# Kernel tuning notes

Hardware: AMD Instinct MI355X
Metric: run time of the kernel (lower is better)

## Reference

```python
import jax, jax.numpy as jnp
import numpy as np

B, S, N, C = 64, 512, 207, 1
H = 256
D = N * C          # flattened node-feature size (input_size * n_nodes)
DIN = 2 * D        # GRU input size with concat_mask=True


def setup_inputs() -> dict:
    key = jax.random.key(0)
    ks = jax.random.split(key, 8)
    x = jax.random.normal(ks[0], (B, S, N, C), dtype=jnp.float32)
    mask = (jax.random.uniform(ks[1], (B, S, N, C)) < 0.8).astype(jnp.float32)
    bnd = 1.0 / np.sqrt(H)  # torch default init bound for GRUCell and Linear(H, D)
    u = lambda k, shp: jax.random.uniform(k, shp, minval=-bnd, maxval=bnd, dtype=jnp.float32)
    return {
        'x': x,
        'mask': mask,
        'W_ih': u(ks[2], (3 * H, DIN)),
        'W_hh': u(ks[3], (3 * H, H)),
        'b_ih': u(ks[4], (3 * H,)),
        'b_hh': u(ks[5], (3 * H,)),
        'W_ro': u(ks[6], (D, H)),
        'b_ro': u(ks[7], (D,)),
    }


def _gru_cell(x_t, h, W_ih, W_hh, b_ih, b_hh):
    gi = x_t @ W_ih.T + b_ih              # [B, 3H]
    gh = h @ W_hh.T + b_hh                # [B, 3H]
    i_r, i_z, i_n = jnp.split(gi, 3, axis=-1)
    h_r, h_z, h_n = jnp.split(gh, 3, axis=-1)
    r = jax.nn.sigmoid(i_r + h_r)
    z = jax.nn.sigmoid(i_z + h_z)
    n = jnp.tanh(i_n + r * h_n)
    return (1.0 - z) * n + z * h


def reference(x, mask, W_ih, W_hh, b_ih, b_hh, W_ro, b_ro):
    b, s, n_nodes, c = x.shape
    xf = x.reshape(b, s, n_nodes * c)       # 'b s n c -> b s (n c)'
    mf = mask.reshape(b, s, n_nodes * c)
    h0 = jnp.zeros((b, H), dtype=x.dtype)   # state_init='zero'
    xhat0 = h0 @ W_ro.T + b_ro              # readout of initial state

    def step(carry, inp):
        h, x_hat = carry
        x_t, m_t = inp                       # [B, D] each
        x_p = jnp.where(m_t > 0.5, x_t, x_hat)
        x_in = jnp.concatenate([x_p, m_t], axis=-1)  # concat_mask
        h_new = _gru_cell(x_in, h, W_ih, W_hh, b_ih, b_hh)
        x_hat_new = h_new @ W_ro.T + b_ro
        return (h_new, x_hat_new), x_hat_new

    # scan over steps 0..S-2, time axis leading
    xs = (jnp.swapaxes(xf[:, :-1], 0, 1), jnp.swapaxes(mf[:, :-1], 0, 1))
    _, preds = jax.lax.scan(step, (h0, xhat0), xs)           # [S-1, B, D]
    preds = jnp.concatenate([xhat0[None], preds], axis=0)    # [S, B, D]
    x_hat = jnp.swapaxes(preds, 0, 1).reshape(b, s, n_nodes, c)
    return x_hat
```

## Files before the change

kernel.cpp:

```cpp
#include <hip/hip_runtime.h>
#include <math.h>

#define BB 64
#define SS 512
#define DD 207
#define HH 256
#define NWG 64
#define LDW 676
#define ROW 260
#define AG __HIP_MEMORY_SCOPE_AGENT

#define SROWS 672
#define HOFF  416
#define SLOT  (SROWS * 64)
#define BUF_FLOATS ((size_t)SS * SLOT)
#define FLAG_U32 (64 * 32)
#define STAGE_FLOATS ((size_t)SS * DD * 64)
#define WS_NEED6 ((BUF_FLOATS + FLAG_U32 + STAGE_FLOATS) * sizeof(float))

#define V3_AROWS 928
#define V3_HBASE 416
#define V3_ACT (V3_AROWS * 64)
#define V3_FLAGS (64 * 32)
#define V3_WS_SMALL ((size_t)(V3_ACT + V3_FLAGS) * sizeof(float))
#define V3_WS_FULL  ((size_t)(V3_ACT + V3_FLAGS + STAGE_FLOATS) * sizeof(float))

__device__ __forceinline__ void ast4(float* p, float v) {
    union { float f; unsigned u; } c; c.f = v;
    __hip_atomic_store((unsigned*)p, c.u, __ATOMIC_RELAXED, AG);
}

__device__ __forceinline__ void run_range6(
    const float4* __restrict__ A4, const float* __restrict__ wgl,
    float* __restrict__ red, int u, int bp, int wc0, int gr0, int len, int slot)
{
    float4 c0 = make_float4(0.f, 0.f, 0.f, 0.f);
    float4 c1 = c0, c2 = c0;
    #pragma unroll 4
    for (int k = 0; k < len; k += 4) {
        float4 a0 = A4[(gr0 + k + 0) * 16 + bp];
        float4 a1 = A4[(gr0 + k + 1) * 16 + bp];
        float4 a2 = A4[(gr0 + k + 2) * 16 + bp];
        float4 a3 = A4[(gr0 + k + 3) * 16 + bp];
        float4 w0 = *(const float4*)&wgl[(0 + u) * LDW + wc0 + k];
        float4 w1 = *(const float4*)&wgl[(4 + u) * LDW + wc0 + k];
        float4 w2 = *(const float4*)&wgl[(8 + u) * LDW + wc0 + k];
        c0.x += a0.x*w0.x + a1.x*w0.y + a2.x*w0.z + a3.x*w0.w;
        c0.y += a0.y*w0.x + a1.y*w0.y + a2.y*w0.z + a3.y*w0.w;
        c0.z += a0.z*w0.x + a1.z*w0.y + a2.z*w0.z + a3.z*w0.w;
        c0.w += a0.w*w0.x + a1.w*w0.y + a2.w*w0.z + a3.w*w0.w;
        c1.x += a0.x*w1.x + a1.x*w1.y + a2.x*w1.z + a3.x*w1.w;
        c1.y += a0.y*w1.x + a1.y*w1.y + a2.y*w1.z + a3.y*w1.w;
        c1.z += a0.z*w1.x + a1.z*w1.y + a2.z*w1.z + a3.z*w1.w;
        c1.w += a0.w*w1.x + a1.w*w1.y + a2.w*w1.z + a3.w*w1.w;
        c2.x += a0.x*w2.x + a1.x*w2.y + a2.x*w2.z + a3.x*w2.w;
        c2.y += a0.y*w2.x + a1.y*w2.y + a2.y*w2.z + a3.y*w2.w;
        c2.z += a0.z*w2.x + a1.z*w2.y + a2.z*w2.z + a3.z*w2.w;
        c2.w += a0.w*w2.x + a1.w*w2.y + a2.w*w2.z + a3.w*w2.w;
    }
    float4* R4 = (float4*)red;
    R4[(slot * 12 + 0 + u) * 16 + bp] = c0;
    R4[(slot * 12 + 4 + u) * 16 + bp] = c1;
    R4[(slot * 12 + 8 + u) * 16 + bp] = c2;
}

__global__ __launch_bounds__(256) void rnn_init6(float* __restrict__ ws) {
    int i = blockIdx.x * blockDim.x + threadIdx.x;
    for (int idx = i; idx < HH * 64; idx += gridDim.x * blockDim.x)
        ws[HOFF * 64 + idx] = 0.f;
    unsigned* fl = (unsigned*)(ws + BUF_FLOATS);
    for (int idx = i; idx < FLAG_U32; idx += gridDim.x * blockDim.x)
        fl[idx] = 0u;
}

__global__ __launch_bounds__(512) void rnn_persist7(
    const float* __restrict__ x, const float* __restrict__ mask,
    const float* __restrict__ W_ih, const float* __restrict__ W_hh,
    const float* __restrict__ b_ih, const float* __restrict__ b_hh,
    const float* __restrict__ W_ro, const float* __restrict__ b_ro,
    float* __restrict__ ws, float* __restrict__ out)
{
    const int wg = blockIdx.x;
    const int tid = threadIdx.x;
    const int lane = tid & 63;
    const int wv = tid >> 6;

    float* buf = ws;
    unsigned* flags = (unsigned*)(ws + BUF_FLOATS);
    float* stage = ws + BUF_FLOATS + FLAG_U32;

    __shared__ float wgl[12 * LDW];
    __shared__ float wrol[4 * ROW];
    __shared__ float red[16 * 12 * 64];
    __shared__ float redB[32 * 64];
    __shared__ float hloc[4 * 64];
    __shared__ float bihl[12], bhhl[12], brol[4];

    const int d0 = (207 * wg) / NWG;
    const int d1 = (207 * (wg + 1)) / NWG;
    const int dc = d1 - d0;

    for (int i = tid; i < 12 * LDW; i += 512) {
        int r = i / LDW, c = i - r * LDW;
        int rg = (r >> 2) * 256 + wg * 4 + (r & 3);
        float v = 0.f;
        if (c < 414) v = W_ih[rg * 414 + c];
        else if (c >= 416 && c < 672) v = W_hh[rg * 256 + (c - 416)];
        wgl[i] = v;
    }
    for (int i = tid; i < 4 * 256; i += 512) {
        int dl_ = i >> 8, j = i & 255;
        wrol[dl_ * ROW + j] = (dl_ < dc) ? W_ro[(d0 + dl_) * 256 + j] : 0.f;
    }
    if (tid < 12) {
        int rg = (tid >> 2) * 256 + wg * 4 + (tid & 3);
        bihl[tid] = b_ih[rg];
        bhhl[tid] = b_hh[rg];
    }
    if (tid < 4) brol[tid] = (tid < dc) ? b_ro[d0 + tid] : 0.f;
    if (tid < 256) hloc[tid] = 0.f;
    __syncthreads();

    const float4* A4 = (const float4*)buf;
    const int u  = lane >> 4;
    const int bp = lane & 15;

    const bool have = (tid < dc * 64);
    const int dl = tid >> 6, b = tid & 63;
    const size_t gbase = (size_t)b * (SS * DD) + (d0 + dl);
    float xv_pf = 0.f, mv_pf = 0.f;
    if (have) { xv_pf = x[gbase]; mv_pf = mask[gbase]; }

    unsigned gen = 0;

    for (int t = 0; t < SS; ++t) {
        const int sbase = t * SROWS;

        {
            const float* hrow = buf + (size_t)(sbase + HOFF) * 64;
            const int jb = wv * 32;
            float acc0 = 0.f, acc1 = 0.f, acc2 = 0.f, acc3 = 0.f;
            #pragma unroll 4
            for (int j = 0; j < 32; j += 4) {
                float a0 = hrow[(jb + j + 0) * 64 + lane];
                float a1 = hrow[(jb + j + 1) * 64 + lane];
                float a2 = hrow[(jb + j + 2) * 64 + lane];
                float a3 = hrow[(jb + j + 3) * 64 + lane];
                float4 w0 = *(const float4*)&wrol[0 * ROW + jb + j];
                float4 w1 = *(const float4*)&wrol[1 * ROW + jb + j];
                float4 w2 = *(const float4*)&wrol[2 * ROW + jb + j];
                float4 w3 = *(const float4*)&wrol[3 * ROW + jb + j];
                acc0 += a0*w0.x + a1*w0.y + a2*w0.z + a3*w0.w;
                acc1 += a0*w1.x + a1*w1.y + a2*w1.z + a3*w1.w;
                acc2 += a0*w2.x + a1*w2.y + a2*w2.z + a3*w2.w;
                acc3 += a0*w3.x + a1*w3.y + a2*w3.z + a3*w3.w;
            }
            redB[(wv * 4 + 0) * 64 + lane] = acc0;
            redB[(wv * 4 + 1) * 64 + lane] = acc1;
            redB[(wv * 4 + 2) * 64 + lane] = acc2;
            redB[(wv * 4 + 3) * 64 + lane] = acc3;
        }
        __syncthreads();
        if (have) {
            float xh = brol[dl];
            #pragma unroll
            for (int g = 0; g < 8; ++g)
                xh += redB[(g * 4 + dl) * 64 + b];
            stage[(t * DD + d0 + dl) * 64 + b] = xh;
            if (t < SS - 1) {
                float xi = (mv_pf > 0.5f) ? xv_pf : xh;
                ast4(&buf[(size_t)(sbase + d0 + dl) * 64 + b], xi);
                ast4(&buf[(size_t)(sbase + 207 + d0 + dl) * 64 + b], mv_pf);
            }
        }
        if (t == SS - 1) break;

        ++gen;
        asm volatile("s_waitcnt vmcnt(0)" ::: "memory");
        __syncthreads();
        if (tid == 0)
            __hip_atomic_store(&flags[wg * 32], gen, __ATOMIC_RELAXED, AG);

        run_range6(A4, wgl, red, u, bp, 416 + wv * 32, sbase + HOFF + wv * 32, 32, 8 + wv);

        if (tid < 64) {
            unsigned* f = &flags[tid * 32];
            while (__hip_atomic_load(f, __ATOMIC_RELAXED, AG) < gen) {}
        }
        __syncthreads();

        run_range6(A4, wgl, red, u, bp, wv * 52, sbase + wv * 52, 52, wv);
        __syncthreads();

        if (tid < 256) {
            const int u2 = tid >> 6, b2 = tid & 63;
            float gir = bihl[0 + u2], giz = bihl[4 + u2], gin = bihl[8 + u2];
            float ghr = bhhl[0 + u2], ghz = bhhl[4 + u2], ghn = bhhl[8 + u2];
            #pragma unroll
            for (int s = 0; s < 8; ++s) {
                gir += red[(s * 12 + 0 + u2) * 64 + b2];
                giz += red[(s * 12 + 4 + u2) * 64 + b2];
                gin += red[(s * 12 + 8 + u2) * 64 + b2];
                ghr += red[((8 + s) * 12 + 0 + u2) * 64 + b2];
                ghz += red[((8 + s) * 12 + 4 + u2) * 64 + b2];
                ghn += red[((8 + s) * 12 + 8 + u2) * 64 + b2];
            }
            float r = 1.f / (1.f + __expf(-(gir + ghr)));
            float z = 1.f / (1.f + __expf(-(giz + ghz)));
            float n = tanhf(gin + r * ghn);
            float hn = (1.f - z) * n + z * hloc[u2 * 64 + b2];
            hloc[u2 * 64 + b2] = hn;
            ast4(&buf[(size_t)((t + 1) * SROWS + HOFF + wg * 4 + u2) * 64 + b2], hn);
        }

        ++gen;
        asm volatile("s_waitcnt vmcnt(0)" ::: "memory");
        __syncthreads();
        if (tid == 0)
            __hip_atomic_store(&flags[wg * 32], gen, __ATOMIC_RELAXED, AG);

        if (have && t + 1 < SS - 1) {
            xv_pf = x[gbase + (size_t)(t + 1) * DD];
            mv_pf = mask[gbase + (size_t)(t + 1) * DD];
        }

        if (tid < 64) {
            unsigned* f = &flags[tid * 32];
            while (__hip_atomic_load(f, __ATOMIC_RELAXED, AG) < gen) {}
        }
        __syncthreads();
    }
}

__global__ __launch_bounds__(256) void out_transpose(
    const float* __restrict__ stage, float* __restrict__ out)
{
    __shared__ float lds[DD * 65];
    const int t = blockIdx.x;
    const float* st = stage + (size_t)t * DD * 64;
    for (int i = threadIdx.x; i < DD * 64; i += 256) {
        int d = i >> 6, b = i & 63;
        lds[d * 65 + b] = st[i];
    }
    __syncthreads();
    for (int i = threadIdx.x; i < DD * 64; i += 256) {
        int b = i / DD, d = i - b * DD;
        out[(size_t)b * (SS * DD) + (size_t)t * DD + d] = lds[d * 65 + b];
    }
}

__device__ __forceinline__ void v3_gbar(unsigned* flags, int wg, unsigned g) {
    __syncthreads();
    if (threadIdx.x < 64) {
        if (threadIdx.x == 0) {
            __builtin_amdgcn_fence(__ATOMIC_RELEASE, "agent");
            __hip_atomic_store(&flags[wg * 32], g, __ATOMIC_RELAXED, AG);
        }
        unsigned* f = &flags[threadIdx.x * 32];
        while (__hip_atomic_load(f, __ATOMIC_RELAXED, AG) < g) { }
        __builtin_amdgcn_fence(__ATOMIC_ACQUIRE, "agent");
    }
    __syncthreads();
}

__global__ __launch_bounds__(256) void v3_init(float* __restrict__ ws) {
    int i = blockIdx.x * blockDim.x + threadIdx.x;
    const int nz = (672 - 414) * 64;
    for (int idx = i; idx < nz; idx += gridDim.x * blockDim.x)
        ws[414 * 64 + idx] = 0.f;
    for (int idx = i; idx < V3_FLAGS; idx += gridDim.x * blockDim.x)
        ((unsigned*)(ws + V3_ACT))[idx] = 0u;
}

template<bool STAGE>
__global__ __launch_bounds__(256) void v3_persist(
    const float* __restrict__ x, const float* __restrict__ mask,
    const float* __restrict__ W_ih, const float* __restrict__ W_hh,
    const float* __restrict__ b_ih, const float* __restrict__ b_hh,
    const float* __restrict__ W_ro, const float* __restrict__ b_ro,
    float* __restrict__ ws, float* __restrict__ out)
{
    const int wg = blockIdx.x;
    const int tid = threadIdx.x;
    const int lane = tid & 63;
    const int wv = tid >> 6;

    float* actg = ws;
    unsigned* flags = (unsigned*)(ws + V3_ACT);
    float* stage = ws + V3_ACT + V3_FLAGS;

    __shared__ float wgl[12 * LDW];
    __shared__ float wrol[4 * 256];
    __shared__ float red[5 * 12 * 64];
    __shared__ float redB[16 * 64];
    __shared__ float hloc[4 * 64];
    __shared__ float bihl[12], bhhl[12], brol[4];

    const int d0 = (207 * wg) / NWG;
    const int d1 = (207 * (wg + 1)) / NWG;
    const int dc = d1 - d0;

// ... 130 lines not shown
    __syncthreads();
    const float* xb = x + (size_t)b * SS * DD;
    const float* mb = mask + (size_t)b * SS * DD;
    float* ob = out + (size_t)b * SS * DD;
    for (int t = 0; t < SS; ++t) {
        if (tid < DD) ob[t * DD + tid] = xhat[tid];
        if (t == SS - 1) break;
        if (tid < DD) {
            float m = mb[t * DD + tid], xv = xb[t * DD + tid];
            xin[tid] = (m > 0.5f) ? xv : xhat[tid];
            xin[DD + tid] = m;
        }
        __syncthreads();
        float accI = bih, accH = bhh;
        const float* wi = W_ih + (size_t)tid * 414;
        for (int k = 0; k < 414; ++k) accI += wi[k] * xin[k];
        const float* wh = W_hh + (size_t)tid * HH;
        for (int k = 0; k < HH; ++k) accH += wh[k] * h[k];
        gi[tid] = accI; gh[tid] = accH;
        __syncthreads();
        if (tid < HH) {
            float r = 1.f / (1.f + __expf(-(gi[tid] + gh[tid])));
            float z = 1.f / (1.f + __expf(-(gi[HH + tid] + gh[HH + tid])));
            float n = tanhf(gi[2 * HH + tid] + r * gh[2 * HH + tid]);
            hnew[tid] = (1.f - z) * n + z * h[tid];
        }
        __syncthreads();
        if (tid < DD) {
            float acc = bro;
            const float* wr = W_ro + (size_t)tid * HH;
            for (int k = 0; k < HH; ++k) acc += wr[k] * hnew[k];
            xhat[tid] = acc;
        }
        if (tid < HH) h[tid] = hnew[tid];
        __syncthreads();
    }
}

extern "C" void kernel_launch(void* const* d_in, const int* in_sizes, int n_in,
                              void* d_out, int out_size, void* d_ws, size_t ws_size,
                              hipStream_t stream) {
    const float* x    = (const float*)d_in[0];
    const float* mask = (const float*)d_in[1];
    const float* W_ih = (const float*)d_in[2];
    const float* W_hh = (const float*)d_in[3];
    const float* b_ih = (const float*)d_in[4];
    const float* b_hh = (const float*)d_in[5];
    const float* W_ro = (const float*)d_in[6];
    const float* b_ro = (const float*)d_in[7];
    float* out = (float*)d_out;
    float* ws  = (float*)d_ws;

    if (ws_size >= WS_NEED6) {
        hipLaunchKernelGGL(rnn_init6, dim3(64), dim3(256), 0, stream, ws);
        hipLaunchKernelGGL(rnn_persist7, dim3(NWG), dim3(512), 0, stream,
                           x, mask, W_ih, W_hh, b_ih, b_hh, W_ro, b_ro, ws, out);
        hipLaunchKernelGGL(out_transpose, dim3(SS), dim3(256), 0, stream,
                           ws + BUF_FLOATS + FLAG_U32, out);
    } else if (ws_size >= V3_WS_FULL) {
        hipLaunchKernelGGL(v3_init, dim3(32), dim3(256), 0, stream, ws);
        hipLaunchKernelGGL((v3_persist<true>), dim3(NWG), dim3(256), 0, stream,
                           x, mask, W_ih, W_hh, b_ih, b_hh, W_ro, b_ro, ws, out);
        hipLaunchKernelGGL(out_transpose, dim3(SS), dim3(256), 0, stream,
                           ws + V3_ACT + V3_FLAGS, out);
    } else if (ws_size >= V3_WS_SMALL) {
        hipLaunchKernelGGL(v3_init, dim3(32), dim3(256), 0, stream, ws);
        hipLaunchKernelGGL((v3_persist<false>), dim3(NWG), dim3(256), 0, stream,
                           x, mask, W_ih, W_hh, b_ih, b_hh, W_ro, b_ro, ws, out);
    } else {
        hipLaunchKernelGGL(rnn_fallback, dim3(BB), dim3(768), 0, stream,
                           x, mask, W_ih, W_hh, b_ih, b_hh, W_ro, b_ro, out);
    }
}
```

Baseline: 5.100 ms.

## Split batch into two half-groups with separate flags to overlap grid barriers

Replaces the persistent GRU kernel with a version that splits the 64-sample batch into two 32-sample groups, each with its own activation buffer and its own flag generation. While one group waits on its grid-wide flag barrier, the workgroup computes the other group's readout or GEMV, so barrier latency is hidden behind useful work. It also splits K across lanes (ks) and rebalances the input-GEMV ranges per wave. The cost is twice as many barrier rounds per step and smaller per-barrier work, plus more intricate ordering between the two groups.

```diff
diff --git a/kernel.cpp b/kernel.cpp
--- a/kernel.cpp
+++ b/kernel.cpp
@@ -6,14 +6,14 @@
 #define DD 207
 #define HH 256
 #define NWG 64
+#define GB 32
 #define LDW 676
 #define ROW 260
 #define AG __HIP_MEMORY_SCOPE_AGENT
 
 #define SROWS 672
 #define HOFF  416
-#define SLOT  (SROWS * 64)
-#define BUF_FLOATS ((size_t)SS * SLOT)
+#define BUF_FLOATS ((size_t)SS * 2 * SROWS * GB)
 #define FLAG_U32 (64 * 32)
 #define STAGE_FLOATS ((size_t)SS * DD * 64)
 #define WS_NEED6 ((BUF_FLOATS + FLAG_U32 + STAGE_FLOATS) * sizeof(float))
@@ -28,6 +28,329 @@
 __device__ __forceinline__ void ast4(float* p, float v) {
     union { float f; unsigned u; } c; c.f = v;
     __hip_atomic_store((unsigned*)p, c.u, __ATOMIC_RELAXED, AG);
+}
+
+__device__ __forceinline__ void run_range32(
+    const float4* __restrict__ A4, const float* __restrict__ wgl,
+    float* __restrict__ red, int u, int ks, int bp,
+    int wc0, size_t gr0, int len, int slot)
+{
+    float4 c0 = make_float4(0.f, 0.f, 0.f, 0.f);
+    float4 c1 = c0, c2 = c0;
+    const int ko = ks * 4;
+    #pragma unroll 4
+    for (int k = 0; k < len; k += 8) {
+        size_t r = (gr0 + k + ko) * 8 + bp;
+        float4 a0 = A4[r + 0 * 8];
+        float4 a1 = A4[r + 1 * 8];
+        float4 a2 = A4[r + 2 * 8];
+        float4 a3 = A4[r + 3 * 8];
+        const int wc = wc0 + k + ko;
+        float4 w0 = *(const float4*)&wgl[(0 + u) * LDW + wc];
+        float4 w1 = *(const float4*)&wgl[(4 + u) * LDW + wc];
+        float4 w2 = *(const float4*)&wgl[(8 + u) * LDW + wc];
+        c0.x += a0.x*w0.x + a1.x*w0.y + a2.x*w0.z + a3.x*w0.w;
+        c0.y += a0.y*w0.x + a1.y*w0.y + a2.y*w0.z + a3.y*w0.w;
+        c0.z += a0.z*w0.x + a1.z*w0.y + a2.z*w0.z + a3.z*w0.w;
+        c0.w += a0.w*w0.x + a1.w*w0.y + a2.w*w0.z + a3.w*w0.w;
+        c1.x += a0.x*w1.x + a1.x*w1.y + a2.x*w1.z + a3.x*w1.w;
+        c1.y += a0.y*w1.x + a1.y*w1.y + a2.y*w1.z + a3.y*w1.w;
+        c1.z += a0.z*w1.x + a1.z*w1.y + a2.z*w1.z + a3.z*w1.w;
+        c1.w += a0.w*w1.x + a1.w*w1.y + a2.w*w1.z + a3.w*w1.w;
+        c2.x += a0.x*w2.x + a1.x*w2.y + a2.x*w2.z + a3.x*w2.w;
+        c2.y += a0.y*w2.x + a1.y*w2.y + a2.y*w2.z + a3.y*w2.w;
+        c2.z += a0.z*w2.x + a1.z*w2.y + a2.z*w2.z + a3.z*w2.w;
+        c2.w += a0.w*w2.x + a1.w*w2.y + a2.w*w2.z + a3.w*w2.w;
+    }
+    float4* R4 = (float4*)red;
+    const int hs = slot * 2 + ks;
+    R4[(hs * 12 + 0 + u) * 8 + bp] = c0;
+    R4[(hs * 12 + 4 + u) * 8 + bp] = c1;
+    R4[(hs * 12 + 8 + u) * 8 + bp] = c2;
+}
+
+__device__ __forceinline__ void phaseB32(
+    const float* __restrict__ hrow, const float* __restrict__ wrol,
+    float* __restrict__ redB, int wv, int pks, int pb)
+{
+    const int jb = wv * 32 + pks * 16;
+    float acc0 = 0.f, acc1 = 0.f, acc2 = 0.f, acc3 = 0.f;
+    #pragma unroll
+    for (int j = 0; j < 16; j += 4) {
+        float a0 = hrow[(jb + j + 0) * GB + pb];
+        float a1 = hrow[(jb + j + 1) * GB + pb];
+        float a2 = hrow[(jb + j + 2) * GB + pb];
+        float a3 = hrow[(jb + j + 3) * GB + pb];
+        float4 w0 = *(const float4*)&wrol[0 * ROW + jb + j];
+        float4 w1 = *(const float4*)&wrol[1 * ROW + jb + j];
+        float4 w2 = *(const float4*)&wrol[2 * ROW + jb + j];
+        float4 w3 = *(const float4*)&wrol[3 * ROW + jb + j];
+        acc0 += a0*w0.x + a1*w0.y + a2*w0.z + a3*w0.w;
+        acc1 += a0*w1.x + a1*w1.y + a2*w1.z + a3*w1.w;
+        acc2 += a0*w2.x + a1*w2.y + a2*w2.z + a3*w2.w;
+        acc3 += a0*w3.x + a1*w3.y + a2*w3.z + a3*w3.w;
+    }
+    const int hs = wv * 2 + pks;
+    redB[(hs * 4 + 0) * GB + pb] = acc0;
+    redB[(hs * 4 + 1) * GB + pb] = acc1;
+    redB[(hs * 4 + 2) * GB + pb] = acc2;
+    redB[(hs * 4 + 3) * GB + pb] = acc3;
+}
+
+__global__ __launch_bounds__(256) void rnn_init10(float* __restrict__ ws) {
+    int i = blockIdx.x * blockDim.x + threadIdx.x;
+    for (int idx = i; idx < 2 * HH * GB; idx += gridDim.x * blockDim.x) {
+        int g = idx / (HH * GB);
+        int j = idx - g * (HH * GB);
+        ws[((size_t)(g * SROWS) + HOFF) * GB + j] = 0.f;
+    }
+    unsigned* fl = (unsigned*)(ws + BUF_FLOATS);
+    for (int idx = i; idx < FLAG_U32; idx += gridDim.x * blockDim.x)
+        fl[idx] = 0u;
+}
+
+__global__ __launch_bounds__(512) void rnn_persist10(
+    const float* __restrict__ x, const float* __restrict__ mask,
+    const float* __restrict__ W_ih, const float* __restrict__ W_hh,
+    const float* __restrict__ b_ih, const float* __restrict__ b_hh,
+    const float* __restrict__ W_ro, const float* __restrict__ b_ro,
+    float* __restrict__ ws, float* __restrict__ out)
+{
+    const int wg = blockIdx.x;
+    const int tid = threadIdx.x;
+    const int lane = tid & 63;
+    const int wv = tid >> 6;
+
+    float* buf = ws;
+    unsigned* flags = (unsigned*)(ws + BUF_FLOATS);
+    float* stage = ws + BUF_FLOATS + FLAG_U32;
+
+    __shared__ float wgl[12 * LDW];
+    __shared__ float wrol[4 * ROW];
+    __shared__ float red[32 * 12 * GB];
+    __shared__ float redB[16 * 4 * GB];
+    __shared__ float hloc[2 * 128];
+    __shared__ float bihl[12], bhhl[12], brol[4];
+
+    const int d0 = (207 * wg) / NWG;
+    const int d1 = (207 * (wg + 1)) / NWG;
+    const int dc = d1 - d0;
+
+    for (int i = tid; i < 12 * LDW; i += 512) {
+        int r = i / LDW, c = i - r * LDW;
+        int rg = (r >> 2) * 256 + wg * 4 + (r & 3);
+        float v = 0.f;
+        if (c < 414) v = W_ih[rg * 414 + c];
+        else if (c >= 416 && c < 672) v = W_hh[rg * 256 + (c - 416)];
+        wgl[i] = v;
+    }
+    for (int i = tid; i < 4 * 256; i += 512) {
+        int dl_ = i >> 8, j = i & 255;
+        wrol[dl_ * ROW + j] = (dl_ < dc) ? W_ro[(d0 + dl_) * 256 + j] : 0.f;
+    }
+    if (tid < 12) {
+        int rg = (tid >> 2) * 256 + wg * 4 + (tid & 3);
+        bihl[tid] = b_ih[rg];
+        bhhl[tid] = b_hh[rg];
+    }
+    if (tid < 4) brol[tid] = (tid < dc) ? b_ro[d0 + tid] : 0.f;
+    if (tid < 256) hloc[tid] = 0.f;
+    __syncthreads();
+
+    const float4* A4 = (const float4*)buf;
+    const int u  = lane >> 4;
+    const int ks = (lane >> 3) & 1;
+    const int bp = lane & 7;
+    const int pb_b  = lane & 31;
+    const int pb_ks = lane >> 5;
+
+    const bool have = (tid < dc * 32);
+    const int dl = tid >> 5, bb = tid & 31;
+    const size_t gbaseA = (size_t)bb * (SS * DD) + (d0 + dl);
+    const size_t gbaseB = (size_t)(32 + bb) * (SS * DD) + (d0 + dl);
+    float xvA = 0.f, mvA = 0.f, xvB = 0.f, mvB = 0.f;
+    if (have) {
+        xvA = x[gbaseA]; mvA = mask[gbaseA];
+        xvB = x[gbaseB]; mvB = mask[gbaseB];
+    }
+
+    const int xr0  = (wv < 6) ? wv * 56 : 336 + (wv - 6) * 40;
+    const int xlen = (wv < 6) ? 56 : 40;
+
+    unsigned genA = 0, genB = 0;
+
+    for (int t = 0; t < SS; ++t) {
+        const size_t srowA = (size_t)(t * 2 + 0) * SROWS;
+        const size_t srowB = (size_t)(t * 2 + 1) * SROWS;
+
+        phaseB32(buf + (srowA + HOFF) * GB, wrol, redB, wv, pb_ks, pb_b);
+        __syncthreads();
+        if (have) {
+            float xh = brol[dl];
+            #pragma unroll
+            for (int s = 0; s < 16; ++s) xh += redB[(s * 4 + dl) * GB + bb];
+            stage[(t * DD + d0 + dl) * 64 + bb] = xh;
+            if (t < SS - 1) {
+                float xi = (mvA > 0.5f) ? xvA : xh;
+                ast4(&buf[(srowA + d0 + dl) * GB + bb], xi);
+                ast4(&buf[(srowA + 207 + d0 + dl) * GB + bb], mvA);
+            }
+        }
+        if (t == SS - 1) {
+            if (tid < 64) {
+                unsigned* f = &flags[tid * 32 + 8];
+                while (__hip_atomic_load(f, __ATOMIC_RELAXED, AG) < genB) {}
+            }
+            __syncthreads();
+            phaseB32(buf + (srowB + HOFF) * GB, wrol, redB, wv, pb_ks, pb_b);
+            __syncthreads();
+            if (have) {
+                float xh = brol[dl];
+                #pragma unroll
+                for (int s = 0; s < 16; ++s) xh += redB[(s * 4 + dl) * GB + bb];
+                stage[(t * DD + d0 + dl) * 64 + 32 + bb] = xh;
+            }
+            break;
+        }
+
+        ++genA;
+        asm volatile("s_waitcnt vmcnt(0)" ::: "memory");
+        __syncthreads();
+        if (tid == 0)
+            __hip_atomic_store(&flags[wg * 32 + 0], genA, __ATOMIC_RELAXED, AG);
+
+        if (tid < 64) {
+            unsigned* f = &flags[tid * 32 + 8];
+            while (__hip_atomic_load(f, __ATOMIC_RELAXED, AG) < genB) {}
+        }
+        __syncthreads();
+
+        phaseB32(buf + (srowB + HOFF) * GB, wrol, redB, wv, pb_ks, pb_b);
+        __syncthreads();
+        if (have) {
+            float xh = brol[dl];
+            #pragma unroll
+            for (int s = 0; s < 16; ++s) xh += redB[(s * 4 + dl) * GB + bb];
+            stage[(t * DD + d0 + dl) * 64 + 32 + bb] = xh;
+            float xi = (mvB > 0.5f) ? xvB : xh;
+            ast4(&buf[(srowB + d0 + dl) * GB + bb], xi);
+            ast4(&buf[(srowB + 207 + d0 + dl) * GB + bb], mvB);
+        }
+
+        ++genB;
+        asm volatile("s_waitcnt vmcnt(0)" ::: "memory");
+        __syncthreads();
+        if (tid == 0)
+            __hip_atomic_store(&flags[wg * 32 + 8], genB, __ATOMIC_RELAXED, AG);
+
+        run_range32(A4, wgl, red, u, ks, bp, 416 + wv * 32,
+                    srowA + HOFF + wv * 32, 32, 8 + wv);
+
+        if (tid < 64) {
+            unsigned* f = &flags[tid * 32 + 0];
+            while (__hip_atomic_load(f, __ATOMIC_RELAXED, AG) < genA) {}
+        }
+        __syncthreads();
+
+        run_range32(A4, wgl, red, u, ks, bp, xr0, srowA + xr0, xlen, wv);
+        __syncthreads();
+
+        if (tid < 128) {
+            const int u2 = tid >> 5, b2 = tid & 31;
+            float gir = bihl[0 + u2], giz = bihl[4 + u2], gin = bihl[8 + u2];
+            float ghr = bhhl[0 + u2], ghz = bhhl[4 + u2], ghn = bhhl[8 + u2];
+            #pragma unroll
+            for (int s = 0; s < 16; ++s) {
+                gir += red[(s * 12 + 0 + u2) * GB + b2];
+                giz += red[(s * 12 + 4 + u2) * GB + b2];
+                gin += red[(s * 12 + 8 + u2) * GB + b2];
+                ghr += red[((16 + s) * 12 + 0 + u2) * GB + b2];
+                ghz += red[((16 + s) * 12 + 4 + u2) * GB + b2];
+                ghn += red[((16 + s) * 12 + 8 + u2) * GB + b2];
+            }
+            float r = 1.f / (1.f + __expf(-(gir + ghr)));
+            float z = 1.f / (1.f + __expf(-(giz + ghz)));
+            float n = tanhf(gin + r * ghn);
+            float hn = (1.f - z) * n + z * hloc[u2 * 32 + b2];
+            hloc[u2 * 32 + b2] = hn;
+            ast4(&buf[((size_t)((t + 1) * 2 + 0) * SROWS + HOFF + wg * 4 + u2) * GB + b2], hn);
+        }
+
+        ++genA;
+        asm volatile("s_waitcnt vmcnt(0)" ::: "memory");
+        __syncthreads();
+        if (tid == 0)
+            __hip_atomic_store(&flags[wg * 32 + 0], genA, __ATOMIC_RELAXED, AG);
+
+        run_range32(A4, wgl, red, u, ks, bp, 416 + wv * 32,
+                    srowB + HOFF + wv * 32, 32, 8 + wv);
+
+        if (tid < 64) {
+            unsigned* f = &flags[tid * 32 + 8];
+            while (__hip_atomic_load(f, __ATOMIC_RELAXED, AG) < genB) {}
+        }
+        __syncthreads();
+
+        run_range32(A4, wgl, red, u, ks, bp, xr0, srowB + xr0, xlen, wv);
+        __syncthreads();
+
+        if (tid < 128) {
+            const int u2 = tid >> 5, b2 = tid & 31;
+            float gir = bihl[0 + u2], giz = bihl[4 + u2], gin = bihl[8 + u2];
+            float ghr = bhhl[0 + u2], ghz = bhhl[4 + u2], ghn = bhhl[8 + u2];
+            #pragma unroll
+            for (int s = 0; s < 16; ++s) {
+                gir += red[(s * 12 + 0 + u2) * GB + b2];
+                giz += red[(s * 12 + 4 + u2) * GB + b2];
+                gin += red[(s * 12 + 8 + u2) * GB + b2];
+                ghr += red[((16 + s) * 12 + 0 + u2) * GB + b2];
+                ghz += red[((16 + s) * 12 + 4 + u2) * GB + b2];
+                ghn += red[((16 + s) * 12 + 8 + u2) * GB + b2];
+            }
+            float r = 1.f / (1.f + __expf(-(gir + ghr)));
+            float z = 1.f / (1.f + __expf(-(giz + ghz)));
+            float n = tanhf(gin + r * ghn);
+            float hn = (1.f - z) * n + z * hloc[128 + u2 * 32 + b2];
+            hloc[128 + u2 * 32 + b2] = hn;
+            ast4(&buf[((size_t)((t + 1) * 2 + 1) * SROWS + HOFF + wg * 4 + u2) * GB + b2], hn);
+        }
+
+        ++genB;
+        asm volatile("s_waitcnt vmcnt(0)" ::: "memory");
+        __syncthreads();
+        if (tid == 0)
+            __hip_atomic_store(&flags[wg * 32 + 8], genB, __ATOMIC_RELAXED, AG);
+
+        if (have && t + 1 < SS - 1) {
+            xvA = x[gbaseA + (size_t)(t + 1) * DD];
+            mvA = mask[gbaseA + (size_t)(t + 1) * DD];
+            xvB = x[gbaseB + (size_t)(t + 1) * DD];
+            mvB = mask[gbaseB + (size_t)(t + 1) * DD];
+        }
+
+        if (tid < 64) {
+            unsigned* f = &flags[tid * 32 + 0];
+            while (__hip_atomic_load(f, __ATOMIC_RELAXED, AG) < genA) {}
+        }
+        __syncthreads();
+    }
+}
+
+__global__ __launch_bounds__(256) void out_transpose(
+    const float* __restrict__ stage, float* __restrict__ out)
+{
+    __shared__ float lds[DD * 65];
+    const int t = blockIdx.x;
+    const float* st = stage + (size_t)t * DD * 64;
+    for (int i = threadIdx.x; i < DD * 64; i += 256) {
+        int d = i >> 6, b = i & 63;
+        lds[d * 65 + b] = st[i];
+    }
+    __syncthreads();
+    for (int i = threadIdx.x; i < DD * 64; i += 256) {
+        int b = i / DD, d = i - b * DD;
+        out[(size_t)b * (SS * DD) + (size_t)t * DD + d] = lds[d * 65 + b];
+    }
 }
 
 __device__ __forceinline__ void run_range6(
@@ -62,191 +385,6 @@
     R4[(slot * 12 + 0 + u) * 16 + bp] = c0;
     R4[(slot * 12 + 4 + u) * 16 + bp] = c1;
     R4[(slot * 12 + 8 + u) * 16 + bp] = c2;
-}
-
-__global__ __launch_bounds__(256) void rnn_init6(float* __restrict__ ws) {
-    int i = blockIdx.x * blockDim.x + threadIdx.x;
-    for (int idx = i; idx < HH * 64; idx += gridDim.x * blockDim.x)
-        ws[HOFF * 64 + idx] = 0.f;
-    unsigned* fl = (unsigned*)(ws + BUF_FLOATS);
-    for (int idx = i; idx < FLAG_U32; idx += gridDim.x * blockDim.x)
-        fl[idx] = 0u;
-}
-
-__global__ __launch_bounds__(512) void rnn_persist7(
-    const float* __restrict__ x, const float* __restrict__ mask,
-    const float* __restrict__ W_ih, const float* __restrict__ W_hh,
-    const float* __restrict__ b_ih, const float* __restrict__ b_hh,
-    const float* __restrict__ W_ro, const float* __restrict__ b_ro,
-    float* __restrict__ ws, float* __restrict__ out)
-{
-    const int wg = blockIdx.x;
-    const int tid = threadIdx.x;
-    const int lane = tid & 63;
-    const int wv = tid >> 6;
-
-    float* buf = ws;
-    unsigned* flags = (unsigned*)(ws + BUF_FLOATS);
-    float* stage = ws + BUF_FLOATS + FLAG_U32;
-
-    __shared__ float wgl[12 * LDW];
-    __shared__ float wrol[4 * ROW];
-    __shared__ float red[16 * 12 * 64];
-    __shared__ float redB[32 * 64];
-    __shared__ float hloc[4 * 64];
-    __shared__ float bihl[12], bhhl[12], brol[4];
-
-    const int d0 = (207 * wg) / NWG;
-    const int d1 = (207 * (wg + 1)) / NWG;
-    const int dc = d1 - d0;
-
-    for (int i = tid; i < 12 * LDW; i += 512) {
-        int r = i / LDW, c = i - r * LDW;
-        int rg = (r >> 2) * 256 + wg * 4 + (r & 3);
-        float v = 0.f;
-        if (c < 414) v = W_ih[rg * 414 + c];
-        else if (c >= 416 && c < 672) v = W_hh[rg * 256 + (c - 416)];
-        wgl[i] = v;
-    }
-    for (int i = tid; i < 4 * 256; i += 512) {
-        int dl_ = i >> 8, j = i & 255;
-        wrol[dl_ * ROW + j] = (dl_ < dc) ? W_ro[(d0 + dl_) * 256 + j] : 0.f;
-    }
-    if (tid < 12) {
-        int rg = (tid >> 2) * 256 + wg * 4 + (tid & 3);
-        bihl[tid] = b_ih[rg];
-        bhhl[tid] = b_hh[rg];
-    }
-    if (tid < 4) brol[tid] = (tid < dc) ? b_ro[d0 + tid] : 0.f;
-    if (tid < 256) hloc[tid] = 0.f;
-    __syncthreads();
-
-    const float4* A4 = (const float4*)buf;
-    const int u  = lane >> 4;
-    const int bp = lane & 15;
-
-    const bool have = (tid < dc * 64);
-    const int dl = tid >> 6, b = tid & 63;
-    const size_t gbase = (size_t)b * (SS * DD) + (d0 + dl);
-    float xv_pf = 0.f, mv_pf = 0.f;
-    if (have) { xv_pf = x[gbase]; mv_pf = mask[gbase]; }
-
-    unsigned gen = 0;
-
-    for (int t = 0; t < SS; ++t) {
-        const int sbase = t * SROWS;
-
-        {
-            const float* hrow = buf + (size_t)(sbase + HOFF) * 64;
-            const int jb = wv * 32;
-            float acc0 = 0.f, acc1 = 0.f, acc2 = 0.f, acc3 = 0.f;
-            #pragma unroll 4
-            for (int j = 0; j < 32; j += 4) {
-                float a0 = hrow[(jb + j + 0) * 64 + lane];
-                float a1 = hrow[(jb + j + 1) * 64 + lane];
-                float a2 = hrow[(jb + j + 2) * 64 + lane];
-                float a3 = hrow[(jb + j + 3) * 64 + lane];
-                float4 w0 = *(const float4*)&wrol[0 * ROW + jb + j];
-                float4 w1 = *(const float4*)&wrol[1 * ROW + jb + j];
-                float4 w2 = *(const float4*)&wrol[2 * ROW + jb + j];
-                float4 w3 = *(const float4*)&wrol[3 * ROW + jb + j];
-                acc0 += a0*w0.x + a1*w0.y + a2*w0.z + a3*w0.w;
-                acc1 += a0*w1.x + a1*w1.y + a2*w1.z + a3*w1.w;
-                acc2 += a0*w2.x + a1*w2.y + a2*w2.z + a3*w2.w;
-                acc3 += a0*w3.x + a1*w3.y + a2*w3.z + a3*w3.w;
-            }
-            redB[(wv * 4 + 0) * 64 + lane] = acc0;
-            redB[(wv * 4 + 1) * 64 + lane] = acc1;
-            redB[(wv * 4 + 2) * 64 + lane] = acc2;
-            redB[(wv * 4 + 3) * 64 + lane] = acc3;
-        }
-        __syncthreads();
-        if (have) {
-            float xh = brol[dl];
-            #pragma unroll
-            for (int g = 0; g < 8; ++g)
-                xh += redB[(g * 4 + dl) * 64 + b];
-            stage[(t * DD + d0 + dl) * 64 + b] = xh;
-            if (t < SS - 1) {
-                float xi = (mv_pf > 0.5f) ? xv_pf : xh;
-                ast4(&buf[(size_t)(sbase + d0 + dl) * 64 + b], xi);
-                ast4(&buf[(size_t)(sbase + 207 + d0 + dl) * 64 + b], mv_pf);
-            }
-        }
-        if (t == SS - 1) break;
-
-        ++gen;
-        asm volatile("s_waitcnt vmcnt(0)" ::: "memory");
-        __syncthreads();
-        if (tid == 0)
-            __hip_atomic_store(&flags[wg * 32], gen, __ATOMIC_RELAXED, AG);
-
-        run_range6(A4, wgl, red, u, bp, 416 + wv * 32, sbase + HOFF + wv * 32, 32, 8 + wv);
-
-        if (tid < 64) {
-            unsigned* f = &flags[tid * 32];
-            while (__hip_atomic_load(f, __ATOMIC_RELAXED, AG) < gen) {}
-        }
-        __syncthreads();
-
-        run_range6(A4, wgl, red, u, bp, wv * 52, sbase + wv * 52, 52, wv);
-        __syncthreads();
-
-        if (tid < 256) {
-            const int u2 = tid >> 6, b2 = tid & 63;
-            float gir = bihl[0 + u2], giz = bihl[4 + u2], gin = bihl[8 + u2];
-            float ghr = bhhl[0 + u2], ghz = bhhl[4 + u2], ghn = bhhl[8 + u2];
-            #pragma unroll
-            for (int s = 0; s < 8; ++s) {
-                gir += red[(s * 12 + 0 + u2) * 64 + b2];
-                giz += red[(s * 12 + 4 + u2) * 64 + b2];
-                gin += red[(s * 12 + 8 + u2) * 64 + b2];
-                ghr += red[((8 + s) * 12 + 0 + u2) * 64 + b2];
-                ghz += red[((8 + s) * 12 + 4 + u2) * 64 + b2];
-                ghn += red[((8 + s) * 12 + 8 + u2) * 64 + b2];
-            }
-            float r = 1.f / (1.f + __expf(-(gir + ghr)));
-            float z = 1.f / (1.f + __expf(-(giz + ghz)));
-            float n = tanhf(gin + r * ghn);
-            float hn = (1.f - z) * n + z * hloc[u2 * 64 + b2];
-            hloc[u2 * 64 + b2] = hn;
-            ast4(&buf[(size_t)((t + 1) * SROWS + HOFF + wg * 4 + u2) * 64 + b2], hn);
-        }
-
-        ++gen;
-        asm volatile("s_waitcnt vmcnt(0)" ::: "memory");
-        __syncthreads();
-        if (tid == 0)
-            __hip_atomic_store(&flags[wg * 32], gen, __ATOMIC_RELAXED, AG);
-
-        if (have && t + 1 < SS - 1) {
-            xv_pf = x[gbase + (size_t)(t + 1) * DD];
-            mv_pf = mask[gbase + (size_t)(t + 1) * DD];
-        }
-
-        if (tid < 64) {
-            unsigned* f = &flags[tid * 32];
-            while (__hip_atomic_load(f, __ATOMIC_RELAXED, AG) < gen) {}
-        }
-        __syncthreads();
-    }
-}
-
-__global__ __launch_bounds__(256) void out_transpose(
-    const float* __restrict__ stage, float* __restrict__ out)
-{
-    __shared__ float lds[DD * 65];
-    const int t = blockIdx.x;
-    const float* st = stage + (size_t)t * DD * 64;
-    for (int i = threadIdx.x; i < DD * 64; i += 256) {
-        int d = i >> 6, b = i & 63;
-        lds[d * 65 + b] = st[i];
-    }
-    __syncthreads();
-    for (int i = threadIdx.x; i < DD * 64; i += 256) {
-        int b = i / DD, d = i - b * DD;
-        out[(size_t)b * (SS * DD) + (size_t)t * DD + d] = lds[d * 65 + b];
-    }
 }
 
 __device__ __forceinline__ void v3_gbar(unsigned* flags, int wg, unsigned g) {
@@ -483,8 +621,8 @@
     float* ws  = (float*)d_ws;
 
     if (ws_size >= WS_NEED6) {
-        hipLaunchKernelGGL(rnn_init6, dim3(64), dim3(256), 0, stream, ws);
-        hipLaunchKernelGGL(rnn_persist7, dim3(NWG), dim3(512), 0, stream,
+        hipLaunchKernelGGL(rnn_init10, dim3(64), dim3(256), 0, stream, ws);
+        hipLaunchKernelGGL(rnn_persist10, dim3(NWG), dim3(512), 0, stream,
                            x, mask, W_ih, W_hh, b_ih, b_hh, W_ro, b_ro, ws, out);
         hipLaunchKernelGGL(out_transpose, dim3(SS), dim3(256), 0, stream,
                            ws + BUF_FLOATS + FLAG_U32, out);
```

Measured after the change: 6.915 ms. 1.36x slower.

## Precompute masked input GEMV off critical path and split per-step barrier flags

Applied to the files above, without the earlier changes.

A new pre-pass kernel transposes the inputs into a staged buffer holding mask*x and the mask. The persistent kernel splits the input GEMV algebraically. The known part (masked x and the mask columns) is computed before waiting for the hidden state. Only the (1-m)*x_hat contribution is computed after x_hat is published. Separate flags for the x_hat and h phases replace the shared generation counter, which removes the full barrier at the end of each step. The cost is an extra launch, more workspace and more LDS for the reduction buffer.

```diff
diff --git a/kernel.cpp b/kernel.cpp
--- a/kernel.cpp
+++ b/kernel.cpp
@@ -10,10 +10,10 @@
 #define ROW 260
 #define AG __HIP_MEMORY_SCOPE_AGENT
 
-#define SROWS 672
-#define HOFF  416
-#define SLOT  (SROWS * 64)
-#define BUF_FLOATS ((size_t)SS * SLOT)
+#define IN_ROWS 416
+#define IN_FLOATS ((size_t)SS * IN_ROWS * 64)
+#define HR_FLOATS ((size_t)SS * HH * 64)
+#define BUF_FLOATS (IN_FLOATS + HR_FLOATS)
 #define FLAG_U32 (64 * 32)
 #define STAGE_FLOATS ((size_t)SS * DD * 64)
 #define WS_NEED6 ((BUF_FLOATS + FLAG_U32 + STAGE_FLOATS) * sizeof(float))
@@ -64,16 +64,112 @@
     R4[(slot * 12 + 8 + u) * 16 + bp] = c2;
 }
 
-__global__ __launch_bounds__(256) void rnn_init6(float* __restrict__ ws) {
+__device__ __forceinline__ void gemvX(
+    const float4* __restrict__ S4, const float4* __restrict__ IN4,
+    const float* __restrict__ wgl, float* __restrict__ red,
+    int u, int bp, int t, int r0, int nrow, int slot)
+{
+    float4 c0 = make_float4(0.f, 0.f, 0.f, 0.f);
+    float4 c1 = c0, c2 = c0;
+    const int sb = t * DD + r0;
+    const int mb = t * IN_ROWS + 207 + r0;
+    int k = 0;
+    for (; k + 4 <= nrow; k += 4) {
+        float4 s0 = S4[(sb + k + 0) * 16 + bp];
+        float4 s1 = S4[(sb + k + 1) * 16 + bp];
+        float4 s2 = S4[(sb + k + 2) * 16 + bp];
+        float4 s3 = S4[(sb + k + 3) * 16 + bp];
+        float4 m0 = IN4[(mb + k + 0) * 16 + bp];
+        float4 m1 = IN4[(mb + k + 1) * 16 + bp];
+        float4 m2 = IN4[(mb + k + 2) * 16 + bp];
+        float4 m3 = IN4[(mb + k + 3) * 16 + bp];
+        float4 a0, a1, a2, a3;
+        a0.x = fmaf(-m0.x, s0.x, s0.x); a0.y = fmaf(-m0.y, s0.y, s0.y);
+        a0.z = fmaf(-m0.z, s0.z, s0.z); a0.w = fmaf(-m0.w, s0.w, s0.w);
+        a1.x = fmaf(-m1.x, s1.x, s1.x); a1.y = fmaf(-m1.y, s1.y, s1.y);
+        a1.z = fmaf(-m1.z, s1.z, s1.z); a1.w = fmaf(-m1.w, s1.w, s1.w);
+        a2.x = fmaf(-m2.x, s2.x, s2.x); a2.y = fmaf(-m2.y, s2.y, s2.y);
+        a2.z = fmaf(-m2.z, s2.z, s2.z); a2.w = fmaf(-m2.w, s2.w, s2.w);
+        a3.x = fmaf(-m3.x, s3.x, s3.x); a3.y = fmaf(-m3.y, s3.y, s3.y);
+        a3.z = fmaf(-m3.z, s3.z, s3.z); a3.w = fmaf(-m3.w, s3.w, s3.w);
+        const int wc = r0 + k;
+        float4 w0 = *(const float4*)&wgl[(0 + u) * LDW + wc];
+        float4 w1 = *(const float4*)&wgl[(4 + u) * LDW + wc];
+        float4 w2 = *(const float4*)&wgl[(8 + u) * LDW + wc];
+        c0.x += a0.x*w0.x + a1.x*w0.y + a2.x*w0.z + a3.x*w0.w;
+        c0.y += a0.y*w0.x + a1.y*w0.y + a2.y*w0.z + a3.y*w0.w;
+        c0.z += a0.z*w0.x + a1.z*w0.y + a2.z*w0.z + a3.z*w0.w;
+        c0.w += a0.w*w0.x + a1.w*w0.y + a2.w*w0.z + a3.w*w0.w;
+        c1.x += a0.x*w1.x + a1.x*w1.y + a2.x*w1.z + a3.x*w1.w;
+        c1.y += a0.y*w1.x + a1.y*w1.y + a2.y*w1.z + a3.y*w1.w;
+        c1.z += a0.z*w1.x + a1.z*w1.y + a2.z*w1.z + a3.z*w1.w;
+        c1.w += a0.w*w1.x + a1.w*w1.y + a2.w*w1.z + a3.w*w1.w;
+        c2.x += a0.x*w2.x + a1.x*w2.y + a2.x*w2.z + a3.x*w2.w;
+        c2.y += a0.y*w2.x + a1.y*w2.y + a2.y*w2.z + a3.y*w2.w;
+        c2.z += a0.z*w2.x + a1.z*w2.y + a2.z*w2.z + a3.z*w2.w;
+        c2.w += a0.w*w2.x + a1.w*w2.y + a2.w*w2.z + a3.w*w2.w;
+    }
+    for (; k < nrow; ++k) {
+        float4 s = S4[(sb + k) * 16 + bp];
+        float4 m = IN4[(mb + k) * 16 + bp];
+        float4 a;
+        a.x = fmaf(-m.x, s.x, s.x); a.y = fmaf(-m.y, s.y, s.y);
+        a.z = fmaf(-m.z, s.z, s.z); a.w = fmaf(-m.w, s.w, s.w);
+        float w0 = wgl[(0 + u) * LDW + r0 + k];
+        float w1 = wgl[(4 + u) * LDW + r0 + k];
+        float w2 = wgl[(8 + u) * LDW + r0 + k];
+        c0.x += a.x*w0; c0.y += a.y*w0; c0.z += a.z*w0; c0.w += a.w*w0;
+        c1.x += a.x*w1; c1.y += a.y*w1; c1.z += a.z*w1; c1.w += a.w*w1;
+        c2.x += a.x*w2; c2.y += a.y*w2; c2.z += a.z*w2; c2.w += a.w*w2;
+    }
+    float4* R4 = (float4*)red;
+    R4[(slot * 12 + 0 + u) * 16 + bp] = c0;
+    R4[(slot * 12 + 4 + u) * 16 + bp] = c1;
+    R4[(slot * 12 + 8 + u) * 16 + bp] = c2;
+}
+
+__global__ __launch_bounds__(256) void stage_inputs(
+    const float* __restrict__ x, const float* __restrict__ mask,
+    float* __restrict__ ws)
+{
+    __shared__ float lds[DD * 65];
+    const int t = blockIdx.x;
+    float* IN = ws;
+    for (int i = threadIdx.x; i < DD * 64; i += 256) {
+        int b = i / DD, d = i - b * DD;
+        size_t g = (size_t)b * (SS * DD) + (size_t)t * DD + d;
+        float xv = x[g], mv = mask[g];
+        lds[d * 65 + b] = (mv > 0.5f) ? xv : 0.f;
+    }
+    __syncthreads();
+    for (int i = threadIdx.x; i < DD * 64; i += 256) {
+        int d = i >> 6, b = i & 63;
+        IN[((size_t)t * IN_ROWS + d) * 64 + b] = lds[d * 65 + b];
+    }
+    __syncthreads();
+    for (int i = threadIdx.x; i < DD * 64; i += 256) {
+        int b = i / DD, d = i - b * DD;
+        lds[d * 65 + b] = mask[(size_t)b * (SS * DD) + (size_t)t * DD + d];
+    }
+    __syncthreads();
+    for (int i = threadIdx.x; i < DD * 64; i += 256) {
+        int d = i >> 6, b = i & 63;
+        IN[((size_t)t * IN_ROWS + 207 + d) * 64 + b] = lds[d * 65 + b];
+    }
+    for (int i = threadIdx.x; i < 2 * 64; i += 256)
+        IN[((size_t)t * IN_ROWS + 414) * 64 + i] = 0.f;
+}
+
+__global__ __launch_bounds__(256) void rnn_init11(float* __restrict__ ws) {
     int i = blockIdx.x * blockDim.x + threadIdx.x;
     for (int idx = i; idx < HH * 64; idx += gridDim.x * blockDim.x)
-        ws[HOFF * 64 + idx] = 0.f;
+        ws[IN_FLOATS + idx] = 0.f;
     unsigned* fl = (unsigned*)(ws + BUF_FLOATS);
     for (int idx = i; idx < FLAG_U32; idx += gridDim.x * blockDim.x)
         fl[idx] = 0u;
 }
 
-__global__ __launch_bounds__(512) void rnn_persist7(
+__global__ __launch_bounds__(512) void rnn_persist11(
     const float* __restrict__ x, const float* __restrict__ mask,
     const float* __restrict__ W_ih, const float* __restrict__ W_hh,
     const float* __restrict__ b_ih, const float* __restrict__ b_hh,
@@ -85,13 +181,18 @@
     const int lane = tid & 63;
     const int wv = tid >> 6;
 
-    float* buf = ws;
+    float* INf = ws;
+    float* HRf = ws + IN_FLOATS;
     unsigned* flags = (unsigned*)(ws + BUF_FLOATS);
     float* stage = ws + BUF_FLOATS + FLAG_U32;
 
+    const float4* IN4 = (const float4*)INf;
+    const float4* HR4 = (const float4*)HRf;
+    const float4* S4  = (const float4*)stage;
+
     __shared__ float wgl[12 * LDW];
     __shared__ float wrol[4 * ROW];
-    __shared__ float red[16 * 12 * 64];
+    __shared__ float red[24 * 12 * 64];
     __shared__ float redB[32 * 64];
     __shared__ float hloc[4 * 64];
     __shared__ float bihl[12], bhhl[12], brol[4];
@@ -121,23 +222,30 @@
     if (tid < 256) hloc[tid] = 0.f;
     __syncthreads();
 
-    const float4* A4 = (const float4*)buf;
     const int u  = lane >> 4;
     const int bp = lane & 15;
 
     const bool have = (tid < dc * 64);
     const int dl = tid >> 6, b = tid & 63;
-    const size_t gbase = (size_t)b * (SS * DD) + (d0 + dl);
-    float xv_pf = 0.f, mv_pf = 0.f;
-    if (have) { xv_pf = x[gbase]; mv_pf = mask[gbase]; }
-
-    unsigned gen = 0;
+
+    const int xr0  = wv * 28;
+    const int xlen = (wv < 7) ? 28 : 11;
+
+    unsigned genX = 0, genH = 0;
 
     for (int t = 0; t < SS; ++t) {
-        const int sbase = t * SROWS;
+        if (t < SS - 1)
+            run_range6(IN4, wgl, red, u, bp, wv * 52,
+                       t * IN_ROWS + wv * 52, 52, wv);
+
+        if (tid < 64) {
+            unsigned* f = &flags[tid * 32 + 8];
+            while (__hip_atomic_load(f, __ATOMIC_RELAXED, AG) < genH) {}
+        }
+        __syncthreads();
 
         {
-            const float* hrow = buf + (size_t)(sbase + HOFF) * 64;
+            const float* hrow = HRf + (size_t)t * HH * 64;
             const int jb = wv * 32;
             float acc0 = 0.f, acc1 = 0.f, acc2 = 0.f, acc3 = 0.f;
             #pragma unroll 4
@@ -161,35 +269,32 @@
             redB[(wv * 4 + 3) * 64 + lane] = acc3;
         }
         __syncthreads();
+
         if (have) {
             float xh = brol[dl];
             #pragma unroll
             for (int g = 0; g < 8; ++g)
                 xh += redB[(g * 4 + dl) * 64 + b];
-            stage[(t * DD + d0 + dl) * 64 + b] = xh;
-            if (t < SS - 1) {
-                float xi = (mv_pf > 0.5f) ? xv_pf : xh;
-                ast4(&buf[(size_t)(sbase + d0 + dl) * 64 + b], xi);
-                ast4(&buf[(size_t)(sbase + 207 + d0 + dl) * 64 + b], mv_pf);
-            }
+            ast4(&stage[((size_t)t * DD + d0 + dl) * 64 + b], xh);
         }
         if (t == SS - 1) break;
 
-        ++gen;
+        ++genX;
         asm volatile("s_waitcnt vmcnt(0)" ::: "memory");
         __syncthreads();
         if (tid == 0)
-            __hip_atomic_store(&flags[wg * 32], gen, __ATOMIC_RELAXED, AG);
-
-        run_range6(A4, wgl, red, u, bp, 416 + wv * 32, sbase + HOFF + wv * 32, 32, 8 + wv);
+            __hip_atomic_store(&flags[wg * 32 + 0], genX, __ATOMIC_RELAXED, AG);
+
+        run_range6(HR4, wgl, red, u, bp, 416 + wv * 32,
+                   t * HH + wv * 32, 32, 8 + wv);
 
         if (tid < 64) {
-            unsigned* f = &flags[tid * 32];
-            while (__hip_atomic_load(f, __ATOMIC_RELAXED, AG) < gen) {}
-        }
-        __syncthreads();
-
-        run_range6(A4, wgl, red, u, bp, wv * 52, sbase + wv * 52, 52, wv);
+            unsigned* f = &flags[tid * 32 + 0];
+            while (__hip_atomic_load(f, __ATOMIC_RELAXED, AG) < genX) {}
+        }
+        __syncthreads();
+
+        gemvX(S4, IN4, wgl, red, u, bp, t, xr0, xlen, 16 + wv);
         __syncthreads();
 
         if (tid < 256) {
@@ -198,9 +303,12 @@
             float ghr = bhhl[0 + u2], ghz = bhhl[4 + u2], ghn = bhhl[8 + u2];
             #pragma unroll
             for (int s = 0; s < 8; ++s) {
-                gir += red[(s * 12 + 0 + u2) * 64 + b2];
-                giz += red[(s * 12 + 4 + u2) * 64 + b2];
-                gin += red[(s * 12 + 8 + u2) * 64 + b2];
+                gir += red[(s * 12 + 0 + u2) * 64 + b2]
+                     + red[((16 + s) * 12 + 0 + u2) * 64 + b2];
+                giz += red[(s * 12 + 4 + u2) * 64 + b2]
+                     + red[((16 + s) * 12 + 4 + u2) * 64 + b2];
+                gin += red[(s * 12 + 8 + u2) * 64 + b2]
+                     + red[((16 + s) * 12 + 8 + u2) * 64 + b2];
                 ghr += red[((8 + s) * 12 + 0 + u2) * 64 + b2];
                 ghz += red[((8 + s) * 12 + 4 + u2) * 64 + b2];
                 ghn += red[((8 + s) * 12 + 8 + u2) * 64 + b2];
@@ -210,25 +318,14 @@
             float n = tanhf(gin + r * ghn);
             float hn = (1.f - z) * n + z * hloc[u2 * 64 + b2];
             hloc[u2 * 64 + b2] = hn;
-            ast4(&buf[(size_t)((t + 1) * SROWS + HOFF + wg * 4 + u2) * 64 + b2], hn);
-        }
-
-        ++gen;
+            ast4(&HRf[((size_t)(t + 1) * HH + wg * 4 + u2) * 64 + b2], hn);
+        }
+
+        ++genH;
         asm volatile("s_waitcnt vmcnt(0)" ::: "memory");
         __syncthreads();
         if (tid == 0)
-            __hip_atomic_store(&flags[wg * 32], gen, __ATOMIC_RELAXED, AG);
-
-        if (have && t + 1 < SS - 1) {
-            xv_pf = x[gbase + (size_t)(t + 1) * DD];
-            mv_pf = mask[gbase + (size_t)(t + 1) * DD];
-        }
-
-        if (tid < 64) {
-            unsigned* f = &flags[tid * 32];
-            while (__hip_atomic_load(f, __ATOMIC_RELAXED, AG) < gen) {}
-        }
-        __syncthreads();
+            __hip_atomic_store(&flags[wg * 32 + 8], genH, __ATOMIC_RELAXED, AG);
     }
 }
 
@@ -483,8 +580,10 @@
     float* ws  = (float*)d_ws;
 
     if (ws_size >= WS_NEED6) {
-        hipLaunchKernelGGL(rnn_init6, dim3(64), dim3(256), 0, stream, ws);
-        hipLaunchKernelGGL(rnn_persist7, dim3(NWG), dim3(512), 0, stream,
+        hipLaunchKernelGGL(stage_inputs, dim3(SS), dim3(256), 0, stream,
+                           x, mask, ws);
+        hipLaunchKernelGGL(rnn_init11, dim3(64), dim3(256), 0, stream, ws);
+        hipLaunchKernelGGL(rnn_persist11, dim3(NWG), dim3(512), 0, stream,
                            x, mask, W_ih, W_hh, b_ih, b_hh, W_ro, b_ro, ws, out);
         hipLaunchKernelGGL(out_transpose, dim3(SS), dim3(256), 0, stream,
                            ws + BUF_FLOATS + FLAG_U32, out);
```

After: 6.697 ms. +31.3%, slower.

## Precompute mask half of input projection one step ahead during barrier wait

Applied to the files above, without the earlier changes.

The mask half of the W_ih input projection depends only on the mask, not on the recurrent state. The kernel now loads x and mask two steps ahead and writes the next step's mask rows to the shared buffer early. It then computes that step's mask-column contribution into a separate reduction slot while waiting on the second grid-wide flag barrier. The critical-path input GEMV shrinks to roughly the x-columns plus the mask boundary column, rebalanced across waves, at the cost of more LDS for the reduction and more complex step bookkeeping.

```diff
diff --git a/kernel.cpp b/kernel.cpp
--- a/kernel.cpp
+++ b/kernel.cpp
@@ -73,7 +73,7 @@
         fl[idx] = 0u;
 }
 
-__global__ __launch_bounds__(512) void rnn_persist7(
+__global__ __launch_bounds__(512) void rnn_persist12(
     const float* __restrict__ x, const float* __restrict__ mask,
     const float* __restrict__ W_ih, const float* __restrict__ W_hh,
     const float* __restrict__ b_ih, const float* __restrict__ b_hh,
@@ -91,7 +91,7 @@
 
     __shared__ float wgl[12 * LDW];
     __shared__ float wrol[4 * ROW];
-    __shared__ float red[16 * 12 * 64];
+    __shared__ float red[24 * 12 * 64];
     __shared__ float redB[32 * 64];
     __shared__ float hloc[4 * 64];
     __shared__ float bihl[12], bhhl[12], brol[4];
@@ -119,6 +119,8 @@
     }
     if (tid < 4) brol[tid] = (tid < dc) ? b_ro[d0 + tid] : 0.f;
     if (tid < 256) hloc[tid] = 0.f;
+    for (int i = tid; i < 8 * 12 * 64; i += 512)
+        red[16 * 12 * 64 + i] = 0.f;
     __syncthreads();
 
     const float4* A4 = (const float4*)buf;
@@ -128,8 +130,15 @@
     const bool have = (tid < dc * 64);
     const int dl = tid >> 6, b = tid & 63;
     const size_t gbase = (size_t)b * (SS * DD) + (d0 + dl);
-    float xv_pf = 0.f, mv_pf = 0.f;
-    if (have) { xv_pf = x[gbase]; mv_pf = mask[gbase]; }
+
+    float xva = 0.f, mva = 0.f, xvb = 0.f, mvb = 0.f;
+    if (have) {
+        xva = x[gbase];      mva = mask[gbase];
+        xvb = x[gbase + DD]; mvb = mask[gbase + DD];
+    }
+
+    const int cr0  = (wv < 4) ? wv * 28 : 112 + (wv - 4) * 24;
+    const int clen = (wv < 4) ? 28 : 24;
 
     unsigned gen = 0;
 
@@ -168,9 +177,10 @@
                 xh += redB[(g * 4 + dl) * 64 + b];
             stage[(t * DD + d0 + dl) * 64 + b] = xh;
             if (t < SS - 1) {
-                float xi = (mv_pf > 0.5f) ? xv_pf : xh;
+                float xi = (mva > 0.5f) ? xva : xh;
                 ast4(&buf[(size_t)(sbase + d0 + dl) * 64 + b], xi);
-                ast4(&buf[(size_t)(sbase + 207 + d0 + dl) * 64 + b], mv_pf);
+                if (t < 2)
+                    ast4(&buf[(size_t)(sbase + 207 + d0 + dl) * 64 + b], mva);
             }
         }
         if (t == SS - 1) break;
@@ -189,7 +199,11 @@
         }
         __syncthreads();
 
-        run_range6(A4, wgl, red, u, bp, wv * 52, sbase + wv * 52, 52, wv);
+        if (t < 2) {
+            run_range6(A4, wgl, red, u, bp, wv * 52, sbase + wv * 52, 52, wv);
+        } else {
+            run_range6(A4, wgl, red, u, bp, cr0, sbase + cr0, clen, wv);
+        }
         __syncthreads();
 
         if (tid < 256) {
@@ -198,9 +212,12 @@
             float ghr = bhhl[0 + u2], ghz = bhhl[4 + u2], ghn = bhhl[8 + u2];
             #pragma unroll
             for (int s = 0; s < 8; ++s) {
-                gir += red[(s * 12 + 0 + u2) * 64 + b2];
-                giz += red[(s * 12 + 4 + u2) * 64 + b2];
-                gin += red[(s * 12 + 8 + u2) * 64 + b2];
+                gir += red[(s * 12 + 0 + u2) * 64 + b2]
+                     + red[((16 + s) * 12 + 0 + u2) * 64 + b2];
+                giz += red[(s * 12 + 4 + u2) * 64 + b2]
+                     + red[((16 + s) * 12 + 4 + u2) * 64 + b2];
+                gin += red[(s * 12 + 8 + u2) * 64 + b2]
+                     + red[((16 + s) * 12 + 8 + u2) * 64 + b2];
                 ghr += red[((8 + s) * 12 + 0 + u2) * 64 + b2];
                 ghz += red[((8 + s) * 12 + 4 + u2) * 64 + b2];
                 ghn += red[((8 + s) * 12 + 8 + u2) * 64 + b2];
@@ -219,10 +236,17 @@
         if (tid == 0)
             __hip_atomic_store(&flags[wg * 32], gen, __ATOMIC_RELAXED, AG);
 
-        if (have && t + 1 < SS - 1) {
-            xv_pf = x[gbase + (size_t)(t + 1) * DD];
-            mv_pf = mask[gbase + (size_t)(t + 1) * DD];
-        }
+        float xvc = 0.f, mvc = 0.f;
+        if (have && t + 2 <= SS - 2) {
+            xvc = x[gbase + (size_t)(t + 2) * DD];
+            mvc = mask[gbase + (size_t)(t + 2) * DD];
+            ast4(&buf[(size_t)((t + 2) * SROWS + 207 + d0 + dl) * 64 + b], mvc);
+        }
+        if (t >= 1 && t + 1 <= SS - 2) {
+            run_range6(A4, wgl, red, u, bp, 208 + cr0,
+                       (t + 1) * SROWS + 208 + cr0, clen, 16 + wv);
+        }
+        xva = xvb; mva = mvb; xvb = xvc; mvb = mvc;
 
         if (tid < 64) {
             unsigned* f = &flags[tid * 32];
@@ -484,7 +508,7 @@
 
     if (ws_size >= WS_NEED6) {
         hipLaunchKernelGGL(rnn_init6, dim3(64), dim3(256), 0, stream, ws);
-        hipLaunchKernelGGL(rnn_persist7, dim3(NWG), dim3(512), 0, stream,
+        hipLaunchKernelGGL(rnn_persist12, dim3(NWG), dim3(512), 0, stream,
                            x, mask, W_ih, W_hh, b_ih, b_hh, W_ro, b_ro, ws, out);
         hipLaunchKernelGGL(out_transpose, dim3(SS), dim3(256), 0, stream,
                            ws + BUF_FLOATS + FLAG_U32, out);
```

Result: slower. 6.009 ms (+17.8%).
